# Performance work log

Hardware: AMD Instinct MI355X
Metric: run time of the kernel (lower is better)

## Reference

```python
import jax, jax.numpy as jnp
import numpy as np

B, L, D, H, MAXS = 32, 2048, 1024, 16, 10
DH = D // H

def _ln(x, w, b, eps=1e-5):
    mu = jnp.mean(x, axis=-1, keepdims=True)
    var = jnp.var(x, axis=-1, keepdims=True)
    return (x - mu) * jax.lax.rsqrt(var + eps) * w + b

def setup_inputs() -> dict:
    key = jax.random.key(0)
    ks = jax.random.split(key, 6)
    s = 1.0 / np.sqrt(D)
    return {
        "grid_embeddings": jax.random.normal(ks[0], (B, L, D), dtype=jnp.float32),
        "symbol_queries": jax.random.normal(ks[1], (MAXS, D), dtype=jnp.float32) * 0.02,
        "qn_w": jnp.ones((D,), jnp.float32), "qn_b": jnp.zeros((D,), jnp.float32),
        "in_proj_w": jax.random.uniform(ks[2], (3 * D, D), jnp.float32, -s, s),
        "in_proj_b": jnp.zeros((3 * D,), jnp.float32),
        "out_w": jax.random.uniform(ks[3], (D, D), jnp.float32, -s, s),
        "out_b": jnp.zeros((D,), jnp.float32),
        "on_w": jnp.ones((D,), jnp.float32), "on_b": jnp.zeros((D,), jnp.float32),
        "symbol_position": 3,
    }

def reference(grid_embeddings, symbol_queries, qn_w, qn_b, in_proj_w, in_proj_b,
              out_w, out_b, on_w, on_b, symbol_position):
    Wq, Wk, Wv = in_proj_w[:D], in_proj_w[D:2*D], in_proj_w[2*D:]
    bq, bk, bv = in_proj_b[:D], in_proj_b[D:2*D], in_proj_b[2*D:]
    # query is identical across batch: compute once
    q0 = _ln(symbol_queries[symbol_position], qn_w, qn_b)          # [D]
    q = (q0 @ Wq.T + bq).reshape(H, DH)                             # [H, DH]
    k = (grid_embeddings @ Wk.T + bk).reshape(B, L, H, DH)          # [B, L, H, DH]
    v = (grid_embeddings @ Wv.T + bv).reshape(B, L, H, DH)          # [B, L, H, DH]
    scale = 1.0 / np.sqrt(DH).astype(np.float32)
    scores = jnp.einsum('hd,blhd->bhl', q, k) * scale               # [B, H, L]
    attn = jax.nn.softmax(scores, axis=-1)                          # [B, H, L]
    ctx = jnp.einsum('bhl,blhd->bhd', attn, v).reshape(B, D)        # [B, D]
    pooled = _ln(ctx @ out_w.T + out_b, on_w, on_b)                 # [B, D]
    return pooled, attn[:, :, None, :]                              # [B,H,1,L]
```

## Files before the change

kernel.cpp:

```cpp
#include <hip/hip_runtime.h>
#include <math.h>

#define BB 32
#define LL 2048
#define DD 1024
#define HH 16
#define DHH 64
#define NCK 16
#define CH  128
#define NT  8

#define WS_Q0    0
#define WS_Q     1024
#define WS_R     2048
#define WS_C     18432
#define WS_CTX   19008
#define WS_Y     51776
#define WS_SSUM  84544
#define WS_PART  92736

#define RED_OFF  65536
#define WT_OFF   69632
#define SMEM_BYTES 71680

typedef __attribute__((ext_vector_type(8))) short    bf16x8;
typedef __attribute__((ext_vector_type(4))) float    f32x4;
typedef __attribute__((ext_vector_type(2))) unsigned u32x2;
typedef __attribute__((ext_vector_type(4))) unsigned short u16x4;

#define MFMA(a, b, c) __builtin_amdgcn_mfma_f32_16x16x32_bf16(a, b, c, 0, 0, 0)

__device__ __forceinline__ unsigned short f2bf(float f) {
    unsigned u = __float_as_uint(f);
    return (unsigned short)((u + 0x7FFFu + ((u >> 16) & 1u)) >> 16);
}
__device__ __forceinline__ bf16x8 pack8(float4 a, float4 b) {
    bf16x8 r;
    r[0] = (short)f2bf(a.x); r[1] = (short)f2bf(a.y);
    r[2] = (short)f2bf(a.z); r[3] = (short)f2bf(a.w);
    r[4] = (short)f2bf(b.x); r[5] = (short)f2bf(b.y);
    r[6] = (short)f2bf(b.z); r[7] = (short)f2bf(b.w);
    return r;
}
__device__ __forceinline__ float wave_sum(float v) {
#pragma unroll
    for (int s = 32; s >= 1; s >>= 1) v += __shfl_xor(v, s, 64);
    return v;
}

__global__ void k_q0(const float* __restrict__ sq, const float* __restrict__ qn_w,
                     const float* __restrict__ qn_b, const int* __restrict__ pos,
                     float* __restrict__ ws) {
    const int t = threadIdx.x;
    const float4 x = ((const float4*)(sq + (size_t)pos[0] * DD))[t];
    float s  = x.x + x.y + x.z + x.w;
    float s2 = x.x * x.x + x.y * x.y + x.z * x.z + x.w * x.w;
    __shared__ float rs[4], rs2[4];
    s = wave_sum(s); s2 = wave_sum(s2);
    const int w = t >> 6, lane = t & 63;
    if (lane == 0) { rs[w] = s; rs2[w] = s2; }
    __syncthreads();
    s  = rs[0] + rs[1] + rs[2] + rs[3];
    s2 = rs2[0] + rs2[1] + rs2[2] + rs2[3];
    const float mu  = s * (1.0f / DD);
    const float var = s2 * (1.0f / DD) - mu * mu;
    const float rstd = rsqrtf(var + 1e-5f);
    const float4 w4 = ((const float4*)qn_w)[t];
    const float4 b4 = ((const float4*)qn_b)[t];
    float4 o;
    o.x = (x.x - mu) * rstd * w4.x + b4.x;
    o.y = (x.y - mu) * rstd * w4.y + b4.y;
    o.z = (x.z - mu) * rstd * w4.z + b4.z;
    o.w = (x.w - mu) * rstd * w4.w + b4.w;
    ((float4*)(ws + WS_Q0))[t] = o;
}

__global__ void k_q(const float* __restrict__ ipw, const float* __restrict__ ipb,
                    float* __restrict__ ws) {
    const int w = threadIdx.x >> 6, lane = threadIdx.x & 63;
    const int d = blockIdx.x * 4 + w;
    const float* row = ipw + (size_t)d * DD;
    const float* q0 = ws + WS_Q0;
    float acc = 0.f;
#pragma unroll
    for (int it = 0; it < 4; ++it) {
        float4 a = ((const float4*)row)[lane + 64 * it];
        float4 b = ((const float4*)q0)[lane + 64 * it];
        acc += a.x * b.x + a.y * b.y + a.z * b.z + a.w * b.w;
    }
    acc = wave_sum(acc);
    if (lane == 0) (ws + WS_Q)[d] = acc + ipb[d];
}

__global__ void k_r(const float* __restrict__ ipw, const float* __restrict__ ipb,
                    float* __restrict__ ws) {
    const int h = blockIdx.x >> 2, qa = blockIdx.x & 3;
    const int t = threadIdx.x;
    const int e = qa * 256 + t;
    const float* q = ws + WS_Q;
    const float* wk = ipw + (size_t)(DD + h * DHH) * DD;
    float acc = 0.f;
#pragma unroll 8
    for (int j = 0; j < DHH; ++j)
        acc += q[h * DHH + j] * wk[(size_t)j * DD + e];
    (ws + WS_R)[h * DD + e] = acc * 0.125f;
    if (qa == 0 && t < 64) {
        float p = q[h * DHH + t] * ipb[DD + h * DHH + t];
        p = wave_sum(p);
        if (t == 0) (ws + WS_C)[h] = p * 0.125f;
    }
}

__global__ __launch_bounds__(256, 2)
void k_fused(const float* __restrict__ gr, const float* __restrict__ ws,
             float* __restrict__ attn_e, float* __restrict__ part,
             float* __restrict__ ssum) {
    extern __shared__ char smem[];
    const int b  = blockIdx.x >> 4;
    const int ck = blockIdx.x & 15;
    const int l0 = ck * CH;
    const int t  = threadIdx.x;
    const int wv = t >> 6, lane = t & 63;
    const int c16 = lane & 15, g = lane >> 4;
    const int estrip = wv * 256;

    bf16x8 rpk[8];
#pragma unroll
    for (int ks = 0; ks < 8; ++ks) {
        const float* rp = ws + WS_R + (size_t)c16 * DD + estrip + ks * 32 + g * 8;
        rpk[ks] = pack8(*(const float4*)rp, *(const float4*)(rp + 4));
    }
    const float myc = (ws + WS_C)[c16];

    f32x4 pv[16];
#pragma unroll
    for (int i = 0; i < 16; ++i) pv[i] = (f32x4){0.f, 0.f, 0.f, 0.f};
    float s_acc = 0.f;

    const int srow = wv * 4 + (lane & 3);
    const int scol = (lane >> 2) * 4;
    const float* gbase = gr + ((size_t)(b * LL + l0) + srow) * DD + scol;
    const int wr_base = (lane >> 4) * 512 + wv * 128 + (lane & 3) * 32 +
                        ((lane >> 2) & 3) * 8;

    float4 raw[16];
#pragma unroll
    for (int j = 0; j < 16; ++j) raw[j] = *(const float4*)(gbase + 64 * j);
#pragma unroll
    for (int j = 0; j < 16; ++j) {
        u16x4 p = {f2bf(raw[j].x), f2bf(raw[j].y), f2bf(raw[j].z), f2bf(raw[j].w)};
        *(u16x4*)(smem + wr_base + j * 2048) = p;
    }
#pragma unroll
    for (int j = 0; j < 16; ++j)
        raw[j] = *(const float4*)(gbase + 16 * DD + 64 * j);
    __syncthreads();

#pragma unroll 1
    for (int tt = 0; tt < NT; ++tt) {
        const char* rb = smem + (tt & 1) * 32768;
        f32x4 sa = {0.f, 0.f, 0.f, 0.f};
#pragma unroll
        for (int ks = 0; ks < 8; ++ks) {
            const int e16 = wv * 16 + ks * 2 + (g >> 1);
            const int byt = (e16 * 4 + (c16 >> 2)) * 128 + (c16 & 3) * 32 + (g & 1) * 16;
            bf16x8 a = *(const bf16x8*)(rb + byt);
            sa = MFMA(a, rpk[ks], sa);
        }
        *(f32x4*)(smem + RED_OFF + (wv * 64 + lane) * 16) = sa;
        __syncthreads();
        if (tt < NT - 1) {
            char* wb = smem + ((tt + 1) & 1) * 32768;
#pragma unroll
            for (int j = 0; j < 16; ++j) {
                u16x4 p = {f2bf(raw[j].x), f2bf(raw[j].y), f2bf(raw[j].z), f2bf(raw[j].w)};
                *(u16x4*)(wb + wr_base + j * 2048) = p;
            }
            if (tt < NT - 2) {
                const float* gs = gbase + (size_t)(tt + 2) * 16 * DD;
#pragma unroll
                for (int j = 0; j < 16; ++j)
                    raw[j] = *(const float4*)(gs + 64 * j);
            }
        }
        f32x4 tot = {myc, myc, myc, myc};
#pragma unroll
        for (int w2 = 0; w2 < 4; ++w2)
            tot += *(const f32x4*)(smem + RED_OFF + (w2 * 64 + lane) * 16);
        f32x4 ex;
        ex[0] = __expf(tot[0]); ex[1] = __expf(tot[1]);
        ex[2] = __expf(tot[2]); ex[3] = __expf(tot[3]);
        u16x4 wp = {f2bf(ex[0]), f2bf(ex[1]), f2bf(ex[2]), f2bf(ex[3])};
        *(u16x4*)(smem + WT_OFF + wv * 512 + c16 * 32 + g * 8) = wp;
        if (wv == 0) {
            float* ap = attn_e + ((size_t)b * HH + c16) * LL + l0 + tt * 16 + g * 4;
            *(float4*)ap = make_float4(ex[0], ex[1], ex[2], ex[3]);
        }
        s_acc += ex[0] + ex[1] + ex[2] + ex[3];
        bf16x8 afrag;
        if (g < 2) {
            afrag = *(const bf16x8*)(smem + WT_OFF + wv * 512 + c16 * 32 + g * 16);
        } else {
            afrag = (bf16x8){0, 0, 0, 0, 0, 0, 0, 0};
        }
#pragma unroll
        for (int grp = 0; grp < 4; ++grp) {
            u32x2 q[8];
#pragma unroll
            for (int n2 = 0; n2 < 4; ++n2) {
                const int est = wv * 16 + grp * 4 + n2;
                const unsigned ta = (unsigned)((tt & 1) * 32768 + est * 512 +
                                               (g & 1) * 256 + c16 * 8);
                asm volatile("ds_read_b64_tr_b16 %0, %1"
                             : "=v"(q[n2 * 2]) : "v"(ta));
                asm volatile("ds_read_b64_tr_b16 %0, %1 offset:128"
                             : "=v"(q[n2 * 2 + 1]) : "v"(ta));
            }
            asm volatile("s_waitcnt lgkmcnt(0)" ::: "memory");
            __builtin_amdgcn_sched_barrier(0);
#pragma unroll
            for (int n2 = 0; n2 < 4; ++n2) {
                union { unsigned u[4]; bf16x8 v; } bb;
                bb.u[0] = q[n2 * 2][0];     bb.u[1] = q[n2 * 2][1];
                bb.u[2] = q[n2 * 2 + 1][0]; bb.u[3] = q[n2 * 2 + 1][1];
                pv[grp * 4 + n2] = MFMA(afrag, bb.v, pv[grp * 4 + n2]);
            }
        }
        __syncthreads();
    }
    float sv = s_acc;
    sv += __shfl_xor(sv, 16, 64);
    sv += __shfl_xor(sv, 32, 64);
    if (wv == 0 && lane < 16)
        ssum[((size_t)b * NCK + ck) * HH + c16] = sv;
    float* pp = part + ((size_t)b * NCK + ck) * (HH * DD);
#pragma unroll
    for (int nt = 0; nt < 16; ++nt) {
#pragma unroll
        for (int r2 = 0; r2 < 4; ++r2)
            pp[(size_t)(g * 4 + r2) * DD + estrip + nt * 16 + c16] = pv[nt][r2];
    }
}

__global__ void k_ctx(const float* __restrict__ ipw, const float* __restrict__ ipb,
                      const float* __restrict__ part, const float* __restrict__ ssum,
                      float* __restrict__ attn_e, float* __restrict__ ctx) {
    const int bh = blockIdx.x, b = bh >> 4, h = bh & 15;
    const int t = threadIdx.x, w = t >> 6, lane = t & 63;
    float S = 0.f;
#pragma unroll
    for (int c = 0; c < NCK; ++c) S += ssum[((size_t)b * NCK + c) * HH + h];
    const float inv = 1.0f / S;
    float4* ar = (float4*)(attn_e + (size_t)bh * LL);
#pragma unroll
    for (int i = 0; i < 2; ++i) {
        float4 v = ar[t + 256 * i];
        v.x *= inv; v.y *= inv; v.z *= inv; v.w *= inv;
        ar[t + 256 * i] = v;
    }
    __shared__ float Xl[DD];
    float4 x = {0.f, 0.f, 0.f, 0.f};
#pragma unroll
    for (int c = 0; c < NCK; ++c) {
        float4 p = ((const float4*)(part + ((size_t)b * NCK + c) * (HH * DD) + h * DD))[t];
        x.x += p.x; x.y += p.y; x.z += p.z; x.w += p.w;
    }
    float4 xs = {x.x * inv, x.y * inv, x.z * inv, x.w * inv};
    ((float4*)Xl)[t] = xs;
    __syncthreads();
    for (int jj = 0; jj < 16; ++jj) {
        const int j = w * 16 + jj;
        const float* row = ipw + (size_t)(2 * DD + h * DHH + j) * DD;
        float acc = 0.f;
#pragma unroll
        for (int it = 0; it < 4; ++it) {
            float4 a = ((const float4*)row)[lane + 64 * it];
            float4 p = ((const float4*)Xl)[lane + 64 * it];
            acc += a.x * p.x + a.y * p.y + a.z * p.z + a.w * p.w;
        }
        acc = wave_sum(acc);
        if (lane == 0) ctx[(size_t)b * DD + h * DHH + j] = acc + ipb[2 * DD + h * DHH + j];
    }
}

__global__ void k_y(const float* __restrict__ ow, const float* __restrict__ ob,
                    const float* __restrict__ ctx, float* __restrict__ y) {
    const int blk = blockIdx.x, b = blk >> 4, ch = blk & 15;
    const int t = threadIdx.x, w = t >> 6, lane = t & 63;
    __shared__ float Xl[DD];
    ((float4*)Xl)[t] = ((const float4*)(ctx + (size_t)b * DD))[t];
    __syncthreads();
    for (int jj = 0; jj < 16; ++jj) {
        const int d = ch * 64 + w * 16 + jj;
        const float* row = ow + (size_t)d * DD;
        float acc = 0.f;
#pragma unroll
        for (int it = 0; it < 4; ++it) {
            float4 a = ((const float4*)row)[lane + 64 * it];
            float4 p = ((const float4*)Xl)[lane + 64 * it];
            acc += a.x * p.x + a.y * p.y + a.z * p.z + a.w * p.w;
        }
        acc = wave_sum(acc);
        if (lane == 0) y[(size_t)b * DD + d] = acc + ob[d];
    }
}

__global__ void k_lnout(const float* __restrict__ y, const float* __restrict__ on_w,
                        const float* __restrict__ on_b, float* __restrict__ outp) {
    const int b = blockIdx.x, t = threadIdx.x;
    const float4 x = ((const float4*)(y + (size_t)b * DD))[t];
    float s  = x.x + x.y + x.z + x.w;
    float s2 = x.x * x.x + x.y * x.y + x.z * x.z + x.w * x.w;
    __shared__ float rs[4], rs2[4];
    s = wave_sum(s); s2 = wave_sum(s2);
    const int w = t >> 6, lane = t & 63;
    if (lane == 0) { rs[w] = s; rs2[w] = s2; }
    __syncthreads();
    s  = rs[0] + rs[1] + rs[2] + rs[3];
    s2 = rs2[0] + rs2[1] + rs2[2] + rs2[3];
    const float mu  = s * (1.0f / DD);
    const float var = s2 * (1.0f / DD) - mu * mu;
    const float rstd = rsqrtf(var + 1e-5f);
    const float4 w4 = ((const float4*)on_w)[t];
    const float4 b4 = ((const float4*)on_b)[t];
    float4 o;
    o.x = (x.x - mu) * rstd * w4.x + b4.x;
    o.y = (x.y - mu) * rstd * w4.y + b4.y;
    o.z = (x.z - mu) * rstd * w4.z + b4.z;
    o.w = (x.w - mu) * rstd * w4.w + b4.w;
    ((float4*)(outp + (size_t)b * DD))[t] = o;
}

extern "C" void kernel_launch(void* const* d_in, const int* in_sizes, int n_in,
                              void* d_out, int out_size, void* d_ws, size_t ws_size,
                              hipStream_t stream) {
    const float* gr   = (const float*)d_in[0];
    const float* sq   = (const float*)d_in[1];
    const float* qn_w = (const float*)d_in[2];
    const float* qn_b = (const float*)d_in[3];
    const float* ipw  = (const float*)d_in[4];
    const float* ipb  = (const float*)d_in[5];
    const float* ow   = (const float*)d_in[6];
    const float* ob   = (const float*)d_in[7];
    const float* on_w = (const float*)d_in[8];
    const float* on_b = (const float*)d_in[9];
    const int*   pos  = (const int*)d_in[10];

    float* out  = (float*)d_out;
    float* attn = out + BB * DD;
    float* ws   = (float*)d_ws;

    hipFuncSetAttribute((const void*)k_fused,
                        hipFuncAttributeMaxDynamicSharedMemorySize, SMEM_BYTES);

    k_q0<<<1, 256, 0, stream>>>(sq, qn_w, qn_b, pos, ws);
    k_q<<<256, 256, 0, stream>>>(ipw, ipb, ws);
    k_r<<<64, 256, 0, stream>>>(ipw, ipb, ws);
    k_fused<<<BB * NCK, 256, SMEM_BYTES, stream>>>(gr, ws, attn,
                                                   ws + WS_PART, ws + WS_SSUM);
    k_ctx<<<BB * HH, 256, 0, stream>>>(ipw, ipb, ws + WS_PART, ws + WS_SSUM,
                                       attn, ws + WS_CTX);
    k_y<<<BB * 16, 256, 0, stream>>>(ow, ob, ws + WS_CTX, ws + WS_Y);
    k_lnout<<<BB, 256, 0, stream>>>(ws + WS_Y, on_w, on_b, out);
}
```

Baseline: 114.6 us.

## Fuse query LayerNorm into projection, store partials as bf16, remap grid loads

```diff
diff --git a/kernel.cpp b/kernel.cpp
--- a/kernel.cpp
+++ b/kernel.cpp
@@ -10,7 +10,6 @@
 #define CH  128
 #define NT  8
 
-#define WS_Q0    0
 #define WS_Q     1024
 #define WS_R     2048
 #define WS_C     18432
@@ -34,13 +33,8 @@
     unsigned u = __float_as_uint(f);
     return (unsigned short)((u + 0x7FFFu + ((u >> 16) & 1u)) >> 16);
 }
-__device__ __forceinline__ bf16x8 pack8(float4 a, float4 b) {
-    bf16x8 r;
-    r[0] = (short)f2bf(a.x); r[1] = (short)f2bf(a.y);
-    r[2] = (short)f2bf(a.z); r[3] = (short)f2bf(a.w);
-    r[4] = (short)f2bf(b.x); r[5] = (short)f2bf(b.y);
-    r[6] = (short)f2bf(b.z); r[7] = (short)f2bf(b.w);
-    return r;
+__device__ __forceinline__ float bf2f(unsigned short u) {
+    return __uint_as_float((unsigned)u << 16);
 }
 __device__ __forceinline__ float wave_sum(float v) {
 #pragma unroll
@@ -48,44 +42,43 @@
     return v;
 }
 
-__global__ void k_q0(const float* __restrict__ sq, const float* __restrict__ qn_w,
-                     const float* __restrict__ qn_b, const int* __restrict__ pos,
-                     float* __restrict__ ws) {
+__global__ void k_q(const float* __restrict__ sq, const float* __restrict__ qn_w,
+                    const float* __restrict__ qn_b, const int* __restrict__ pos,
+                    const float* __restrict__ ipw, const float* __restrict__ ipb,
+                    float* __restrict__ ws) {
     const int t = threadIdx.x;
-    const float4 x = ((const float4*)(sq + (size_t)pos[0] * DD))[t];
-    float s  = x.x + x.y + x.z + x.w;
-    float s2 = x.x * x.x + x.y * x.y + x.z * x.z + x.w * x.w;
+    const int w = t >> 6, lane = t & 63;
+    __shared__ float q0s[DD];
     __shared__ float rs[4], rs2[4];
-    s = wave_sum(s); s2 = wave_sum(s2);
-    const int w = t >> 6, lane = t & 63;
-    if (lane == 0) { rs[w] = s; rs2[w] = s2; }
-    __syncthreads();
-    s  = rs[0] + rs[1] + rs[2] + rs[3];
-    s2 = rs2[0] + rs2[1] + rs2[2] + rs2[3];
-    const float mu  = s * (1.0f / DD);
-    const float var = s2 * (1.0f / DD) - mu * mu;
-    const float rstd = rsqrtf(var + 1e-5f);
-    const float4 w4 = ((const float4*)qn_w)[t];
-    const float4 b4 = ((const float4*)qn_b)[t];
-    float4 o;
-    o.x = (x.x - mu) * rstd * w4.x + b4.x;
-    o.y = (x.y - mu) * rstd * w4.y + b4.y;
-    o.z = (x.z - mu) * rstd * w4.z + b4.z;
-    o.w = (x.w - mu) * rstd * w4.w + b4.w;
-    ((float4*)(ws + WS_Q0))[t] = o;
-}
-
-__global__ void k_q(const float* __restrict__ ipw, const float* __restrict__ ipb,
-                    float* __restrict__ ws) {
-    const int w = threadIdx.x >> 6, lane = threadIdx.x & 63;
+    {
+        const float4 x = ((const float4*)(sq + (size_t)pos[0] * DD))[t];
+        float s  = x.x + x.y + x.z + x.w;
+        float s2 = x.x * x.x + x.y * x.y + x.z * x.z + x.w * x.w;
+        s = wave_sum(s); s2 = wave_sum(s2);
+        if (lane == 0) { rs[w] = s; rs2[w] = s2; }
+        __syncthreads();
+        s  = rs[0] + rs[1] + rs[2] + rs[3];
+        s2 = rs2[0] + rs2[1] + rs2[2] + rs2[3];
+        const float mu  = s * (1.0f / DD);
+        const float var = s2 * (1.0f / DD) - mu * mu;
+        const float rstd = rsqrtf(var + 1e-5f);
+        const float4 w4 = ((const float4*)qn_w)[t];
+        const float4 b4 = ((const float4*)qn_b)[t];
+        float4 o;
+        o.x = (x.x - mu) * rstd * w4.x + b4.x;
+        o.y = (x.y - mu) * rstd * w4.y + b4.y;
+        o.z = (x.z - mu) * rstd * w4.z + b4.z;
+        o.w = (x.w - mu) * rstd * w4.w + b4.w;
+        ((float4*)q0s)[t] = o;
+    }
+    __syncthreads();
     const int d = blockIdx.x * 4 + w;
     const float* row = ipw + (size_t)d * DD;
-    const float* q0 = ws + WS_Q0;
     float acc = 0.f;
 #pragma unroll
     for (int it = 0; it < 4; ++it) {
         float4 a = ((const float4*)row)[lane + 64 * it];
-        float4 b = ((const float4*)q0)[lane + 64 * it];
+        float4 b = ((const float4*)q0s)[lane + 64 * it];
         acc += a.x * b.x + a.y * b.y + a.z * b.z + a.w * b.w;
     }
     acc = wave_sum(acc);
@@ -113,7 +106,7 @@
 
 __global__ __launch_bounds__(256, 2)
 void k_fused(const float* __restrict__ gr, const float* __restrict__ ws,
-             float* __restrict__ attn_e, float* __restrict__ part,
+             float* __restrict__ attn_e, unsigned short* __restrict__ part,
              float* __restrict__ ssum) {
     extern __shared__ char smem[];
     const int b  = blockIdx.x >> 4;
@@ -128,7 +121,13 @@
 #pragma unroll
     for (int ks = 0; ks < 8; ++ks) {
         const float* rp = ws + WS_R + (size_t)c16 * DD + estrip + ks * 32 + g * 8;
-        rpk[ks] = pack8(*(const float4*)rp, *(const float4*)(rp + 4));
+        float4 f0 = *(const float4*)rp, f1 = *(const float4*)(rp + 4);
+        bf16x8 r;
+        r[0] = (short)f2bf(f0.x); r[1] = (short)f2bf(f0.y);
+        r[2] = (short)f2bf(f0.z); r[3] = (short)f2bf(f0.w);
+        r[4] = (short)f2bf(f1.x); r[5] = (short)f2bf(f1.y);
+        r[6] = (short)f2bf(f1.z); r[7] = (short)f2bf(f1.w);
+        rpk[ks] = r;
     }
     const float myc = (ws + WS_C)[c16];
 
@@ -137,11 +136,11 @@
     for (int i = 0; i < 16; ++i) pv[i] = (f32x4){0.f, 0.f, 0.f, 0.f};
     float s_acc = 0.f;
 
-    const int srow = wv * 4 + (lane & 3);
-    const int scol = (lane >> 2) * 4;
+    const int srow = wv * 4 + ((lane >> 2) & 3);
+    const int scol = (lane >> 4) * 16 + (lane & 3) * 4;
     const float* gbase = gr + ((size_t)(b * LL + l0) + srow) * DD + scol;
-    const int wr_base = (lane >> 4) * 512 + wv * 128 + (lane & 3) * 32 +
-                        ((lane >> 2) & 3) * 8;
+    const int wr_base = (lane >> 4) * 512 + wv * 128 + ((lane >> 2) & 3) * 32 +
+                        (lane & 3) * 8;
 
     float4 raw[16];
 #pragma unroll
@@ -233,17 +232,18 @@
     sv += __shfl_xor(sv, 32, 64);
     if (wv == 0 && lane < 16)
         ssum[((size_t)b * NCK + ck) * HH + c16] = sv;
-    float* pp = part + ((size_t)b * NCK + ck) * (HH * DD);
+    unsigned short* pp = part + ((size_t)b * NCK + ck) * (HH * DD);
 #pragma unroll
     for (int nt = 0; nt < 16; ++nt) {
 #pragma unroll
         for (int r2 = 0; r2 < 4; ++r2)
-            pp[(size_t)(g * 4 + r2) * DD + estrip + nt * 16 + c16] = pv[nt][r2];
+            pp[(size_t)(g * 4 + r2) * DD + estrip + nt * 16 + c16] = f2bf(pv[nt][r2]);
     }
 }
 
 __global__ void k_ctx(const float* __restrict__ ipw, const float* __restrict__ ipb,
-                      const float* __restrict__ part, const float* __restrict__ ssum,
+                      const unsigned short* __restrict__ part,
+                      const float* __restrict__ ssum,
                       float* __restrict__ attn_e, float* __restrict__ ctx) {
     const int bh = blockIdx.x, b = bh >> 4, h = bh & 15;
     const int t = threadIdx.x, w = t >> 6, lane = t & 63;
@@ -262,8 +262,10 @@
     float4 x = {0.f, 0.f, 0.f, 0.f};
 #pragma unroll
     for (int c = 0; c < NCK; ++c) {
-        float4 p = ((const float4*)(part + ((size_t)b * NCK + c) * (HH * DD) + h * DD))[t];
-        x.x += p.x; x.y += p.y; x.z += p.z; x.w += p.w;
+        u16x4 p = *(const u16x4*)(part + ((size_t)b * NCK + c) * (HH * DD) +
+                                  (size_t)h * DD + t * 4);
+        x.x += bf2f(p[0]); x.y += bf2f(p[1]);
+        x.z += bf2f(p[2]); x.w += bf2f(p[3]);
     }
     float4 xs = {x.x * inv, x.y * inv, x.z * inv, x.w * inv};
     ((float4*)Xl)[t] = xs;
@@ -349,16 +351,16 @@
     float* out  = (float*)d_out;
     float* attn = out + BB * DD;
     float* ws   = (float*)d_ws;
+    unsigned short* part16 = (unsigned short*)(ws + WS_PART);
 
     hipFuncSetAttribute((const void*)k_fused,
                         hipFuncAttributeMaxDynamicSharedMemorySize, SMEM_BYTES);
 
-    k_q0<<<1, 256, 0, stream>>>(sq, qn_w, qn_b, pos, ws);
-    k_q<<<256, 256, 0, stream>>>(ipw, ipb, ws);
+    k_q<<<256, 256, 0, stream>>>(sq, qn_w, qn_b, pos, ipw, ipb, ws);
     k_r<<<64, 256, 0, stream>>>(ipw, ipb, ws);
     k_fused<<<BB * NCK, 256, SMEM_BYTES, stream>>>(gr, ws, attn,
-                                                   ws + WS_PART, ws + WS_SSUM);
-    k_ctx<<<BB * HH, 256, 0, stream>>>(ipw, ipb, ws + WS_PART, ws + WS_SSUM,
+                                                   part16, ws + WS_SSUM);
+    k_ctx<<<BB * HH, 256, 0, stream>>>(ipw, ipb, part16, ws + WS_SSUM,
                                        attn, ws + WS_CTX);
     k_y<<<BB * 16, 256, 0, stream>>>(ow, ob, ws + WS_CTX, ws + WS_Y);
     k_lnout<<<BB, 256, 0, stream>>>(ws + WS_Y, on_w, on_b, out);
```

Result: faster. 102.9 us (-10.2%).
